# Kernel optimization log

Hardware: AMD Instinct MI355X
Metric: run time of the kernel (lower is better)

## Reference

```python
import jax, jax.numpy as jnp
import numpy as np

BN_EPS = 1e-5

def _conv1x1(x, w, b):
    # x: [B,C,H,W], w: [O,C], b: [O]
    return jnp.einsum('bchw,oc->bohw', x, w) + b[None, :, None, None]

def _maxpool2x2(x):
    B, C, H, W = x.shape
    return x.reshape(B, C, H // 2, 2, W // 2, 2).max(axis=(3, 5))

def setup_inputs() -> dict:
    key = jax.random.key(0)
    ks = jax.random.split(key, 6)
    B, C, H, W = 8, 256, 64, 64
    Ci = C // 2  # inter_channels default
    x = jax.random.normal(ks[0], (B, C, H, W), jnp.float32)
    s = lambda k, sh: jax.random.normal(k, sh, jnp.float32) * 0.02
    return {
        'x': x,
        'w_g': s(ks[1], (Ci, C)), 'b_g': jnp.zeros((Ci,), jnp.float32),
        'w_theta': s(ks[2], (Ci, C)), 'b_theta': jnp.zeros((Ci,), jnp.float32),
        'w_phi': s(ks[3], (Ci, C)), 'b_phi': jnp.zeros((Ci,), jnp.float32),
        'w_w': s(ks[4], (C, Ci)), 'b_w': jnp.zeros((C,), jnp.float32),
        'bn_gamma': 1.0 + 0.1 * jax.random.normal(ks[5], (C,), jnp.float32),
        'bn_beta': jnp.zeros((C,), jnp.float32),
    }

def reference(x, w_g, b_g, w_theta, b_theta, w_phi, b_phi, w_w, b_w, bn_gamma, bn_beta):
    B, C, H, W = x.shape
    Ci = w_g.shape[0]
    # projections (sub_sample=True: maxpool 2x2 on g and phi)
    g_x = _maxpool2x2(_conv1x1(x, w_g, b_g)).reshape(B, Ci, -1)          # [B,Ci,M]
    g_x = g_x.transpose(0, 2, 1)                                          # [B,M,Ci]
    theta_x = _conv1x1(x, w_theta, b_theta).reshape(B, Ci, -1)            # [B,Ci,N]
    theta_x = theta_x.transpose(0, 2, 1)                                  # [B,N,Ci]
    phi_x = _maxpool2x2(_conv1x1(x, w_phi, b_phi)).reshape(B, Ci, -1)     # [B,Ci,M]
    # unscaled embedded-Gaussian attention (no 1/sqrt(d), as in source)
    f = jnp.einsum('bnc,bcm->bnm', theta_x, phi_x)                        # [B,N,M]
    f_div_C = jax.nn.softmax(f, axis=-1)
    y = jnp.einsum('bnm,bmc->bnc', f_div_C, g_x)                          # [B,N,Ci]
    y = y.transpose(0, 2, 1).reshape(B, Ci, H, W)
    # W: 1x1 conv + BatchNorm (training mode: batch statistics)
    wy = _conv1x1(y, w_w, b_w)                                            # [B,C,H,W]
    mean = wy.mean(axis=(0, 2, 3), keepdims=True)
    var = wy.var(axis=(0, 2, 3), keepdims=True)
    wy = (wy - mean) * jax.lax.rsqrt(var + BN_EPS)
    wy = wy * bn_gamma[None, :, None, None] + bn_beta[None, :, None, None]
    return wy + x
```

## Files before the change

### kernel.cpp

```cpp
#include <hip/hip_runtime.h>
#include <hip/hip_bf16.h>

#define NB 8
#define NC 256
#define NCI 128
#define NSP 4096
#define NM 1024

typedef float f32x4 __attribute__((ext_vector_type(4)));
typedef float f32x16 __attribute__((ext_vector_type(16)));
typedef short s16x8 __attribute__((ext_vector_type(8)));
typedef unsigned short u16;

#define OFF_XH  (0ull)
#define OFF_XL  (16777216ull)
#define OFF_THT (33554432ull)
#define OFF_PHT (41943040ull)
#define OFF_GP  (44040192ull)
#define OFF_YH  (46137344ull)
#define OFF_YL  (54525952ull)
#define OFF_WY  (0ull)
#define OFF_WBH (62914560ull)
#define OFF_WBL (63111168ull)
#define OFF_WWH (63307776ull)
#define OFF_WWL (63373312ull)
#define OFF_S   (63438848ull)

#define GLL(src, dst) __builtin_amdgcn_global_load_lds( \
    (const __attribute__((address_space(1))) unsigned*)(src), \
    (__attribute__((address_space(3))) unsigned*)(dst), 16, 0, 0)

__device__ __forceinline__ u16 f2bf(float f) {
  union { __hip_bfloat16 h; u16 u; } v;
  v.h = __float2bfloat16(f);
  return v.u;
}
__device__ __forceinline__ float bf2f(u16 u) {
  union { unsigned u; float f; } v;
  v.u = (unsigned)u << 16;
  return v.f;
}
__device__ __forceinline__ u16 bfmax4(u16 a, u16 b, u16 c, u16 d) {
  float v = fmaxf(fmaxf(bf2f(a), bf2f(b)), fmaxf(bf2f(c), bf2f(d)));
  return f2bf(v);
}
__device__ __forceinline__ unsigned cvtpk(float lo, float hi) {
  unsigned r;
  asm volatile("v_cvt_pk_bf16_f32 %0, %1, %2" : "=v"(r) : "v"(lo), "v"(hi));
  return r;
}

__global__ void zero_stats(float* s) { s[threadIdx.x] = 0.f; }

__global__ __launch_bounds__(256) void wcvt(
    const float* __restrict__ wg, const float* __restrict__ wth,
    const float* __restrict__ wph, const float* __restrict__ ww,
    u16* __restrict__ wbh, u16* __restrict__ wbl,
    u16* __restrict__ wwh, u16* __restrict__ wwl)
{
  int idx = blockIdx.x * 256 + threadIdx.x;
  if (idx < 384 * 256) {
    int row = idx >> 8, k = idx & 255;
    float v = row < 128 ? wg[row * 256 + k]
            : row < 256 ? wth[(row - 128) * 256 + k]
                        : wph[(row - 256) * 256 + k];
    u16 h = f2bf(v);
    wbh[idx] = h;
    wbl[idx] = f2bf(v - bf2f(h));
  } else {
    int j = idx - 384 * 256;
    float v = ww[j];
    u16 h = f2bf(v);
    wwh[j] = h;
    wwl[j] = f2bf(v - bf2f(h));
  }
}

__global__ __launch_bounds__(256) void xt_cvt(const float* __restrict__ x,
                                              u16* __restrict__ xh, u16* __restrict__ xl)
{
  __shared__ float t[64 * 68];
  const int n0 = blockIdx.x << 6, c0 = blockIdx.y << 6, b = blockIdx.z;
  const int tid = threadIdx.x;
  const int cl = tid >> 4, n4 = (tid & 15) << 2;
#pragma unroll
  for (int it = 0; it < 4; ++it) {
    int c = it * 16 + cl;
    float4 v = *(const float4*)&x[((size_t)(b * NC + c0 + c)) * NSP + n0 + n4];
    *(float4*)&t[c * 68 + n4] = v;
  }
  __syncthreads();
#pragma unroll
  for (int it = 0; it < 2; ++it) {
    int task = it * 256 + tid;
    int n = task >> 3, cc = (task & 7) << 3;
    u16 oh[8], ol[8];
#pragma unroll
    for (int i = 0; i < 8; ++i) {
      float v = t[(cc + i) * 68 + n];
      oh[i] = f2bf(v);
      ol[i] = f2bf(v - bf2f(oh[i]));
    }
    size_t dst = ((size_t)(b * NSP + n0 + n)) * NC + c0 + cc;
    *(s16x8*)&xh[dst] = *(s16x8*)oh;
    *(s16x8*)&xl[dst] = *(s16x8*)ol;
  }
}

__global__ __launch_bounds__(512, 1) void proj_fused(
    const u16* __restrict__ xh, const u16* __restrict__ xl,
    const u16* __restrict__ wbh, const u16* __restrict__ wbl,
    const float* __restrict__ bg, const float* __restrict__ bth,
    const float* __restrict__ bph,
    u16* __restrict__ thT, u16* __restrict__ phT, u16* __restrict__ gp)
{
  __shared__ char smem[132608];
  u16* xsh = (u16*)smem;
  u16* xsl = (u16*)(smem + 16384);
  u16* wsh = (u16*)(smem + 32768);
  u16* wsl = (u16*)(smem + 81920);
  u16* outl = (u16*)smem;
  float* bias = (float*)(smem + 131072);

  const int b = blockIdx.y, h2 = blockIdx.x;
  const int n0 = h2 << 7;
  const int tid = threadIdx.x;
  const int wave = tid >> 6, lane = tid & 63;
  const int lo16 = lane & 15, hi4 = lane >> 4;
  const int wr = wave >> 1, wc = wave & 1;
  const int obase = wr * 96, nbase = wc * 64;

  if (tid < 384)
    bias[tid] = tid < 128 ? bg[tid] : tid < 256 ? bth[tid - 128] : bph[tid - 256];

  f32x4 acc[6][4];
#pragma unroll
  for (int i = 0; i < 6; ++i)
#pragma unroll
    for (int j = 0; j < 4; ++j) acc[i][j] = (f32x4){0.f, 0.f, 0.f, 0.f};

  for (int step = 0; step < 4; ++step) {
    __syncthreads();
#pragma unroll
    for (int i = 0; i < 2; ++i) {
      int ci = i * 512 + tid;
      int n = ci >> 3, slot = ci & 7;
      size_t rowb = ((size_t)(b * NSP + n0 + n)) * 512 + step * 128 + ((slot ^ (n & 7)) << 4);
      GLL((const char*)xh + rowb, (char*)xsh + (size_t)(i * 512 + (tid & ~63)) * 16);
      GLL((const char*)xl + rowb, (char*)xsl + (size_t)(i * 512 + (tid & ~63)) * 16);
    }
#pragma unroll
    for (int i = 0; i < 6; ++i) {
      int ci = i * 512 + tid;
      int o = ci >> 3, slot = ci & 7;
      size_t rowb = (size_t)o * 512 + step * 128 + ((slot ^ (o & 7)) << 4);
      GLL((const char*)wbh + rowb, (char*)wsh + (size_t)(i * 512 + (tid & ~63)) * 16);
      GLL((const char*)wbl + rowb, (char*)wsl + (size_t)(i * 512 + (tid & ~63)) * 16);
    }
    __syncthreads();

#pragma unroll
    for (int kc = 0; kc < 2; ++kc) {
      const int sl = kc * 4 + hi4;
      s16x8 bfh[4], bfl[4];
#pragma unroll
      for (int fn = 0; fn < 4; ++fn) {
        int n = nbase + fn * 16 + lo16;
        int off = (int)n * 128 + ((sl ^ (n & 7)) << 4);
        bfh[fn] = *(const s16x8*)((const char*)xsh + off);
        bfl[fn] = *(const s16x8*)((const char*)xsl + off);
      }
      __builtin_amdgcn_s_setprio(1);
#pragma unroll
      for (int fo = 0; fo < 6; ++fo) {
        int o = obase + fo * 16 + lo16;
        int off = (int)o * 128 + ((sl ^ (o & 7)) << 4);
        s16x8 afh = *(const s16x8*)((const char*)wsh + off);
        s16x8 afl = *(const s16x8*)((const char*)wsl + off);
#pragma unroll
        for (int fn = 0; fn < 4; ++fn) {
          acc[fo][fn] = __builtin_amdgcn_mfma_f32_16x16x32_bf16(afh, bfh[fn], acc[fo][fn], 0, 0, 0);
          acc[fo][fn] = __builtin_amdgcn_mfma_f32_16x16x32_bf16(afh, bfl[fn], acc[fo][fn], 0, 0, 0);
          acc[fo][fn] = __builtin_amdgcn_mfma_f32_16x16x32_bf16(afl, bfh[fn], acc[fo][fn], 0, 0, 0);
        }
      }
      __builtin_amdgcn_s_setprio(0);
    }
  }

  __syncthreads();
#pragma unroll
  for (int fo = 0; fo < 6; ++fo) {
    int orow = obase + fo * 16 + hi4 * 4;
    f32x4 bv = *(const f32x4*)&bias[orow];
#pragma unroll
    for (int fn = 0; fn < 4; ++fn) {
      int n = nbase + fn * 16 + lo16;
#pragma unroll
      for (int r = 0; r < 4; ++r)
        outl[(orow + r) * 137 + n] = f2bf(acc[fo][fn][r] + bv[r]);
    }
  }
  __syncthreads();

#pragma unroll
  for (int it = 0; it < 4; ++it) {
    int task = it * 512 + tid;
    int n = task >> 4, cc = (task & 15) << 3;
    u16 o[8];
#pragma unroll
    for (int i = 0; i < 8; ++i) o[i] = outl[(128 + cc + i) * 137 + n];
    *(s16x8*)&thT[((size_t)(b * NSP + n0 + n)) * NCI + cc] = *(s16x8*)o;
  }
  {
    int c = tid >> 2, wq = tid & 3;
    u16 o[8];
#pragma unroll
    for (int j = 0; j < 8; ++j) {
      int w2 = wq * 8 + j;
      o[j] = bfmax4(outl[c * 137 + 2 * w2], outl[c * 137 + 2 * w2 + 1],
                    outl[c * 137 + 64 + 2 * w2], outl[c * 137 + 64 + 2 * w2 + 1]);
    }
    *(s16x8*)&gp[((size_t)(b * NCI + c)) * NM + (h2 << 5) + wq * 8] = *(s16x8*)o;
  }
  {
    int w2 = tid >> 4, cc = (tid & 15) << 3;
    u16 o[8];
#pragma unroll
    for (int i = 0; i < 8; ++i) {
      int c = 256 + cc + i;
      o[i] = bfmax4(outl[c * 137 + 2 * w2], outl[c * 137 + 2 * w2 + 1],
                    outl[c * 137 + 64 + 2 * w2], outl[c * 137 + 64 + 2 * w2 + 1]);
    }
    *(s16x8*)&phT[((size_t)(b * NM + (h2 << 5) + w2)) * NCI + cc] = *(s16x8*)o;
  }
}

__global__ __launch_bounds__(512, 2) void attn_mfma(
    const u16* __restrict__ thT, const u16* __restrict__ phT,
    const u16* __restrict__ gP, u16* __restrict__ yh, u16* __restrict__ yl)
{
  __shared__ char smem[131072];

  const int b = blockIdx.y;
  const int n0 = blockIdx.x << 7;
  const int tid = threadIdx.x;
  const int wave = tid >> 6;
  const int qg = wave & 3;
  const int kh = wave >> 2;
  const int lane = tid & 63;
  const int l31 = lane & 31;
  const int hi1 = lane >> 5;
  const int qbase = n0 + (qg << 5);
  const int swl = (l31 & 7) << 4;

  s16x8 thb[8];
  {
    const u16* tr = &thT[((size_t)b * NSP + qbase + l31) * NCI + hi1 * 8];
#pragma unroll
    for (int kc = 0; kc < 8; ++kc) thb[kc] = *(const s16x8*)&tr[kc * 16];
  }

  f32x16 yacc[4];
#pragma unroll
  for (int ct = 0; ct < 4; ++ct) yacc[ct] = (f32x16)0.f;
  float m_i = -3e38f, l_i = 0.f;

  auto stage = [&](int s, int step) {
    char* base = smem + s * 65536;
    const int m0a = step << 6, m0b = (step + 8) << 6;
#pragma unroll
    for (int it = 0; it < 8; ++it) {
      const int rg = it >> 1;
      int r = ((it & 1) << 9) + tid;
      char* dst = base + rg * 16384 + (size_t)(((it & 1) << 9) + (tid & ~63)) * 16;
      if (rg == 0 || rg == 2) {
        int m0 = (rg == 0) ? m0a : m0b;
        int m = r >> 4, cb = (r & 15) << 4;
        const char* src = (const char*)phT + (((size_t)b * NM + m0 + m) << 8) + (cb ^ ((m & 7) << 4));
        GLL(src, dst);
      } else {
        int m0 = (rg == 1) ? m0a : m0b;
        int c = r >> 3, mb = (r & 7) << 4;
        const char* src = (const char*)gP + (((size_t)b * NCI + c) << 11) + m0 * 2 + (mb ^ ((c & 7) << 4));
        GLL(src, dst);
      }
    }
  };

  stage(0, 0);
  __syncthreads();
  int cur = 0;

  for (int step = 0; step < 8; ++step) {
    if (step < 7) stage(cur ^ 1, step + 1);
    const char* ph = smem + cur * 65536 + kh * 32768;
    const char* gg = ph + 16384;

    f32x16 s0 = (f32x16)0.f, s1 = (f32x16)0.f;
    __builtin_amdgcn_s_setprio(1);
#pragma unroll
    for (int kc = 0; kc < 8; ++kc) {
      int cofs = (kc * 32 + hi1 * 16);
      s16x8 a0 = *(const s16x8*)(ph + l31 * 256 + (cofs ^ swl));
      s16x8 a1 = *(const s16x8*)(ph + (32 + l31) * 256 + (cofs ^ swl));
      s0 = __builtin_amdgcn_mfma_f32_32x32x16_bf16(a0, thb[kc], s0, 0, 0, 0);
      s1 = __builtin_amdgcn_mfma_f32_32x32x16_bf16(a1, thb[kc], s1, 0, 0, 0);
    }
    __builtin_amdgcn_s_setprio(0);

    float pm = s0[0];
#pragma unroll
    for (int i = 1; i < 16; ++i) pm = fmaxf(pm, s0[i]);
#pragma unroll
    for (int i = 0; i < 16; ++i) pm = fmaxf(pm, s1[i]);
    pm = fmaxf(pm, __shfl_xor(pm, 32));
    float mn = fmaxf(m_i, pm);
    float sc = __expf(m_i - mn);
    float rs = 0.f;
#pragma unroll
    for (int i = 0; i < 16; ++i) { s0[i] = __expf(s0[i] - mn); rs += s0[i]; }
#pragma unroll
    for (int i = 0; i < 16; ++i) { s1[i] = __expf(s1[i] - mn); rs += s1[i]; }
    rs += __shfl_xor(rs, 32);
    l_i = l_i * sc + rs;
    m_i = mn;
#pragma unroll
    for (int ct = 0; ct < 4; ++ct)
#pragma unroll
      for (int i = 0; i < 16; ++i) yacc[ct][i] *= sc;

    s16x8 pb[4];
#pragma unroll
    for (int km = 0; km < 4; ++km) {
      int r0 = (km & 1) * 8;
      unsigned X0, X1, X2, X3;
      if (km < 2) {
        X0 = cvtpk(s0[r0 + 0], s0[r0 + 1]);
        X1 = cvtpk(s0[r0 + 2], s0[r0 + 3]);
        X2 = cvtpk(s0[r0 + 4], s0[r0 + 5]);
        X3 = cvtpk(s0[r0 + 6], s0[r0 + 7]);
      } else {
        X0 = cvtpk(s1[r0 + 0], s1[r0 + 1]);
        X1 = cvtpk(s1[r0 + 2], s1[r0 + 3]);
        X2 = cvtpk(s1[r0 + 4], s1[r0 + 5]);
        X3 = cvtpk(s1[r0 + 6], s1[r0 + 7]);
      }
      asm volatile("v_permlane32_swap_b32 %0, %1" : "+v"(X0), "+v"(X2));
      asm volatile("v_permlane32_swap_b32 %0, %1" : "+v"(X1), "+v"(X3));
      unsigned d[4] = {X0, X1, X2, X3};
      pb[km] = *(s16x8*)d;
    }

    __builtin_amdgcn_s_setprio(1);
#pragma unroll
    for (int ct = 0; ct < 4; ++ct) {
      const char* grow = gg + (ct * 32 + l31) * 128;
#pragma unroll
      for (int km = 0; km < 4; ++km) {
        s16x8 ga = *(const s16x8*)(grow + ((km * 32 + hi1 * 16) ^ swl));
        yacc[ct] = __builtin_amdgcn_mfma_f32_32x32x16_bf16(ga, pb[km], yacc[ct], 0, 0, 0);
      }
    }
    __builtin_amdgcn_s_setprio(0);

    __syncthreads();
    cur ^= 1;
  }

  float* yx = (float*)smem;
  float* ml = (float*)(smem + 65536);
  const int slot = (qg << 6) + lane;
  if (kh == 1) {
#pragma unroll
    for (int ct = 0; ct < 4; ++ct)
#pragma unroll
      for (int i4 = 0; i4 < 4; ++i4) {
        f32x4 v = {yacc[ct][i4 * 4 + 0], yacc[ct][i4 * 4 + 1],
                   yacc[ct][i4 * 4 + 2], yacc[ct][i4 * 4 + 3]};
        *(f32x4*)((char*)yx + (size_t)(((ct * 4 + i4) << 8) + slot) * 16) = v;
      }
    ml[slot * 2] = m_i;
    ml[slot * 2 + 1] = l_i;
  }
  __syncthreads();
  if (kh == 1) return;

  float m1 = ml[slot * 2], l1 = ml[slot * 2 + 1];
  float mm = fmaxf(m_i, m1);
  float sc0 = __expf(m_i - mm), sc1 = __expf(m1 - mm);
  float inv = 1.f / (l_i * sc0 + l1 * sc1);
  float a0 = sc0 * inv, a1 = sc1 * inv;
#pragma unroll
  for (int ct = 0; ct < 4; ++ct)
#pragma unroll
    for (int i4 = 0; i4 < 4; ++i4) {
      f32x4 v = *(const f32x4*)((const char*)yx + (size_t)(((ct * 4 + i4) << 8) + slot) * 16);
#pragma unroll
      for (int j = 0; j < 4; ++j)
        yacc[ct][i4 * 4 + j] = yacc[ct][i4 * 4 + j] * a0 + v[j] * a1;
    }

  u16* bounce = (u16*)(smem + 67584) + qg * 4224;
  const int qq = lane >> 1, c0 = (lane & 1) << 6;
#pragma unroll
  for (int pass = 0; pass < 2; ++pass) {
#pragma unroll
    for (int ct = 0; ct < 4; ++ct) {
#pragma unroll
      for (int rp = 0; rp < 8; ++rp) {
        int r = rp * 2;
        int c = ct * 32 + (r & 3) + 8 * (r >> 2) + 4 * hi1;
        float v0 = yacc[ct][r], v1 = yacc[ct][r + 1];
        u16 h0 = f2bf(v0), h1 = f2bf(v1);
        u16 w0 = h0, w1 = h1;
        if (pass) { w0 = f2bf(v0 - bf2f(h0)); w1 = f2bf(v1 - bf2f(h1)); }
        *(unsigned*)&bounce[l31 * 132 + c] = (unsigned)w0 | ((unsigned)w1 << 16);
      }
    }
    asm volatile("s_waitcnt lgkmcnt(0)" ::: "memory");
    u16* dst = pass ? yl : yh;
    size_t row = ((size_t)b * NSP + qbase + qq) * NCI + c0;
#pragma unroll
    for (int k = 0; k < 8; ++k)
      *(s16x8*)&dst[row + k * 8] = *(const s16x8*)&bounce[qq * 132 + c0 + k * 8];
    asm volatile("s_waitcnt lgkmcnt(0)" ::: "memory");
  }
}

__global__ __launch_bounds__(512, 1) void conv_w_mfma(
    const u16* __restrict__ yh, const u16* __restrict__ yl,
    const u16* __restrict__ wwh, const u16* __restrict__ wwl,
    const float* __restrict__ bw, float* __restrict__ wy,
    float* __restrict__ s1g, float* __restrict__ s2g)
{
  __shared__ char smem[102400];
  u16* wsh = (u16*)smem;
  u16* wsl = (u16*)(smem + 32768);
  u16* ysh = (u16*)(smem + 65536);
  u16* ysl = (u16*)(smem + 81920);
  float (*sums1)[256] = (float(*)[256])(smem + 98304);
  float (*sums2)[256] = (float(*)[256])(smem + 100352);

  const int b = blockIdx.y, n0 = blockIdx.x << 7;
  const int tid = threadIdx.x;
  const int wave = tid >> 6, lane = tid & 63;
  const int lo16 = lane & 15, hi4 = lane >> 4;
  const int wr = wave >> 1, wc = wave & 1;
  const int obase = wr * 64, nbase = wc * 64;

  f32x4 acc[4][4];
#pragma unroll
  for (int i = 0; i < 4; ++i)
#pragma unroll
    for (int j = 0; j < 4; ++j) acc[i][j] = (f32x4){0.f, 0.f, 0.f, 0.f};

  for (int step = 0; step < 2; ++step) {
    __syncthreads();
#pragma unroll
    for (int i = 0; i < 4; ++i) {
      int ci = i * 512 + tid;
      int o = ci >> 3, slot = ci & 7;
      size_t rowb = (size_t)o * 256 + step * 128 + ((slot ^ (o & 7)) << 4);
      GLL((const char*)wwh + rowb, (char*)wsh + (size_t)(i * 512 + (tid & ~63)) * 16);
      GLL((const char*)wwl + rowb, (char*)wsl + (size_t)(i * 512 + (tid & ~63)) * 16);
    }
#pragma unroll
    for (int i = 0; i < 2; ++i) {
      int ci = i * 512 + tid;
      int n = ci >> 3, slot = ci & 7;
      size_t rowb = ((size_t)(b * NSP + n0 + n)) * 256 + step * 128 + ((slot ^ (n & 7)) << 4);
      GLL((const char*)yh + rowb, (char*)ysh + (size_t)(i * 512 + (tid & ~63)) * 16);
      GLL((const char*)yl + rowb, (char*)ysl + (size_t)(i * 512 + (tid & ~63)) * 16);
    }
    __syncthreads();

#pragma unroll
    for (int kc = 0; kc < 2; ++kc) {
      const int sl = kc * 4 + hi4;
      s16x8 bfh[4], bfl[4];
#pragma unroll
      for (int fn = 0; fn < 4; ++fn) {
        int n = nbase + fn * 16 + lo16;
        int off = (int)n * 128 + ((sl ^ (n & 7)) << 4);
        bfh[fn] = *(const s16x8*)((const char*)ysh + off);
        bfl[fn] = *(const s16x8*)((const char*)ysl + off);
      }
      __builtin_amdgcn_s_setprio(1);
#pragma unroll
      for (int fo = 0; fo < 4; ++fo) {
        int o = obase + fo * 16 + lo16;
        int off = (int)o * 128 + ((sl ^ (o & 7)) << 4);
        s16x8 afh = *(const s16x8*)((const char*)wsh + off);
        s16x8 afl = *(const s16x8*)((const char*)wsl + off);
#pragma unroll
        for (int fn = 0; fn < 4; ++fn) {
          acc[fo][fn] = __builtin_amdgcn_mfma_f32_16x16x32_bf16(afh, bfh[fn], acc[fo][fn], 0, 0, 0);
          acc[fo][fn] = __builtin_amdgcn_mfma_f32_16x16x32_bf16(afh, bfl[fn], acc[fo][fn], 0, 0, 0);
          acc[fo][fn] = __builtin_amdgcn_mfma_f32_16x16x32_bf16(afl, bfh[fn], acc[fo][fn], 0, 0, 0);
        }
      }
      __builtin_amdgcn_s_setprio(0);
    }
  }

#pragma unroll
  for (int fo = 0; fo < 4; ++fo) {
    int orow = obase + fo * 16 + hi4 * 4;
    float bv[4];
#pragma unroll
    for (int r = 0; r < 4; ++r) bv[r] = bw[orow + r];
    float ss[4] = {0.f, 0.f, 0.f, 0.f}, sq[4] = {0.f, 0.f, 0.f, 0.f};
#pragma unroll
    for (int fn = 0; fn < 4; ++fn) {
      int col = n0 + nbase + fn * 16 + lo16;
#pragma unroll
      for (int r = 0; r < 4; ++r) {
        float v = acc[fo][fn][r] + bv[r];
        wy[((size_t)(b * NC) + orow + r) * NSP + col] = v;
        ss[r] += v;
        sq[r] += v * v;
      }
    }
#pragma unroll
    for (int r = 0; r < 4; ++r) {
#pragma unroll
      for (int d = 1; d < 16; d <<= 1) {
        ss[r] += __shfl_xor(ss[r], d);
        sq[r] += __shfl_xor(sq[r], d);
      }
    }
    if (lo16 == 0) {
#pragma unroll
      for (int r = 0; r < 4; ++r) {
        sums1[wc][orow + r] = ss[r];
        sums2[wc][orow + r] = sq[r];
      }
    }
  }
  __syncthreads();
  if (tid < 256) {
    atomicAdd(&s1g[tid], sums1[0][tid] + sums1[1][tid]);
    atomicAdd(&s2g[tid], sums2[0][tid] + sums2[1][tid]);
  }
}

__global__ __launch_bounds__(256) void bn_res4(
    const float* __restrict__ wy, const float* __restrict__ x,
    const float* __restrict__ s1, const float* __restrict__ s2,
    const float* __restrict__ gamma, const float* __restrict__ beta,
    float* __restrict__ out)
{
  int i4 = (blockIdx.x * 256 + threadIdx.x) << 2;
  int c = (i4 >> 12) & 255;
  const float cnt = 1.f / 32768.f;
  float mean = s1[c] * cnt;
  float var = s2[c] * cnt - mean * mean;
  float inv = rsqrtf(var + 1e-5f) * gamma[c];
  float bet = beta[c];
  float4 w = *(const float4*)&wy[i4];
  float4 xv = *(const float4*)&x[i4];
  float4 o;
  o.x = (w.x - mean) * inv + bet + xv.x;
  o.y = (w.y - mean) * inv + bet + xv.y;
  o.z = (w.z - mean) * inv + bet + xv.z;
  o.w = (w.w - mean) * inv + bet + xv.w;
  *(float4*)&out[i4] = o;
}

extern "C" void kernel_launch(void* const* d_in, const int* in_sizes, int n_in,
                              void* d_out, int out_size, void* d_ws, size_t ws_size,
                              hipStream_t stream) {
  const float* x    = (const float*)d_in[0];
  const float* w_g  = (const float*)d_in[1];
  const float* b_g  = (const float*)d_in[2];
  const float* w_th = (const float*)d_in[3];
  const float* b_th = (const float*)d_in[4];
  const float* w_ph = (const float*)d_in[5];
  const float* b_ph = (const float*)d_in[6];
  const float* w_w  = (const float*)d_in[7];
  const float* b_w  = (const float*)d_in[8];
  const float* gam  = (const float*)d_in[9];
  const float* bet  = (const float*)d_in[10];
  float* out = (float*)d_out;
  char* ws = (char*)d_ws;

  u16*   xh  = (u16*)(ws + OFF_XH);
  u16*   xl  = (u16*)(ws + OFF_XL);
  u16*   thT = (u16*)(ws + OFF_THT);
  u16*   phT = (u16*)(ws + OFF_PHT);
  u16*   gp  = (u16*)(ws + OFF_GP);
  u16*   yhb = (u16*)(ws + OFF_YH);
  u16*   ylb = (u16*)(ws + OFF_YL);
  float* wy  = (float*)(ws + OFF_WY);
  u16*   wbh = (u16*)(ws + OFF_WBH);
  u16*   wbl = (u16*)(ws + OFF_WBL);
  u16*   wwh = (u16*)(ws + OFF_WWH);
  u16*   wwl = (u16*)(ws + OFF_WWL);
  float* s1  = (float*)(ws + OFF_S);
  float* s2  = s1 + 256;

  wcvt<<<dim3(512), 256, 0, stream>>>(w_g, w_th, w_ph, w_w, wbh, wbl, wwh, wwl);
  zero_stats<<<dim3(1), 512, 0, stream>>>(s1);
  xt_cvt<<<dim3(64, 4, 8), 256, 0, stream>>>(x, xh, xl);

  proj_fused<<<dim3(32, 8), 512, 0, stream>>>(xh, xl, wbh, wbl, b_g, b_th, b_ph, thT, phT, gp);

  attn_mfma<<<dim3(32, 8), 512, 0, stream>>>(thT, phT, gp, yhb, ylb);

  conv_w_mfma<<<dim3(32, 8), 512, 0, stream>>>(yhb, ylb, wwh, wwl, b_w, wy, s1, s2);

  bn_res4<<<dim3(8192), 256, 0, stream>>>(wy, x, s1, s2, gam, bet, out);
}
```

Baseline: 112.0 us.

## Split attention key range across four waves per query group with tree merge

After: 138.6 us. +23.7%, slower.

```diff
diff --git a/kernel.cpp b/kernel.cpp
--- a/kernel.cpp
+++ b/kernel.cpp
@@ -236,11 +236,11 @@
   }
 }
 
-__global__ __launch_bounds__(512, 2) void attn_mfma(
+__global__ __launch_bounds__(1024, 4) void attn_mfma(
     const u16* __restrict__ thT, const u16* __restrict__ phT,
     const u16* __restrict__ gP, u16* __restrict__ yh, u16* __restrict__ yl)
 {
-  __shared__ char smem[131072];
+  __shared__ char smem[135168];
 
   const int b = blockIdx.y;
   const int n0 = blockIdx.x << 7;
@@ -253,6 +253,7 @@
   const int hi1 = lane >> 5;
   const int qbase = n0 + (qg << 5);
   const int swl = (l31 & 7) << 4;
+  const int gsw = ((l31 >> 1) & 3) << 4;
 
   s16x8 thb[8];
   {
@@ -268,22 +269,19 @@
 
   auto stage = [&](int s, int step) {
     char* base = smem + s * 65536;
-    const int m0a = step << 6, m0b = (step + 8) << 6;
-#pragma unroll
-    for (int it = 0; it < 8; ++it) {
-      const int rg = it >> 1;
-      int r = ((it & 1) << 9) + tid;
-      char* dst = base + rg * 16384 + (size_t)(((it & 1) << 9) + (tid & ~63)) * 16;
-      if (rg == 0 || rg == 2) {
-        int m0 = (rg == 0) ? m0a : m0b;
-        int m = r >> 4, cb = (r & 15) << 4;
+#pragma unroll
+    for (int it = 0; it < 4; ++it) {
+      const int m0 = (it * 8 + step) << 5;
+      char* reg = base + it * 16384;
+      if (tid < 512) {
+        int m = tid >> 4, cb = (tid & 15) << 4;
         const char* src = (const char*)phT + (((size_t)b * NM + m0 + m) << 8) + (cb ^ ((m & 7) << 4));
-        GLL(src, dst);
+        GLL(src, reg + (size_t)(tid & ~63) * 16);
       } else {
-        int m0 = (rg == 1) ? m0a : m0b;
-        int c = r >> 3, mb = (r & 7) << 4;
-        const char* src = (const char*)gP + (((size_t)b * NCI + c) << 11) + m0 * 2 + (mb ^ ((c & 7) << 4));
-        GLL(src, dst);
+        int c2 = tid - 512;
+        int c = c2 >> 2, mb = (c2 & 3) << 4;
+        const char* src = (const char*)gP + (((size_t)b * NCI + c) << 11) + m0 * 2 + (mb ^ (((c >> 1) & 3) << 4));
+        GLL(src, reg + 8192 + (size_t)(c2 & ~63) * 16);
       }
     }
   };
@@ -294,34 +292,27 @@
 
   for (int step = 0; step < 8; ++step) {
     if (step < 7) stage(cur ^ 1, step + 1);
-    const char* ph = smem + cur * 65536 + kh * 32768;
-    const char* gg = ph + 16384;
-
-    f32x16 s0 = (f32x16)0.f, s1 = (f32x16)0.f;
+    const char* ph = smem + cur * 65536 + kh * 16384;
+    const char* gg = ph + 8192;
+
+    f32x16 s0 = (f32x16)0.f;
     __builtin_amdgcn_s_setprio(1);
 #pragma unroll
     for (int kc = 0; kc < 8; ++kc) {
-      int cofs = (kc * 32 + hi1 * 16);
-      s16x8 a0 = *(const s16x8*)(ph + l31 * 256 + (cofs ^ swl));
-      s16x8 a1 = *(const s16x8*)(ph + (32 + l31) * 256 + (cofs ^ swl));
+      s16x8 a0 = *(const s16x8*)(ph + l31 * 256 + ((kc * 32 + hi1 * 16) ^ swl));
       s0 = __builtin_amdgcn_mfma_f32_32x32x16_bf16(a0, thb[kc], s0, 0, 0, 0);
-      s1 = __builtin_amdgcn_mfma_f32_32x32x16_bf16(a1, thb[kc], s1, 0, 0, 0);
     }
     __builtin_amdgcn_s_setprio(0);
 
     float pm = s0[0];
 #pragma unroll
     for (int i = 1; i < 16; ++i) pm = fmaxf(pm, s0[i]);
-#pragma unroll
-    for (int i = 0; i < 16; ++i) pm = fmaxf(pm, s1[i]);
     pm = fmaxf(pm, __shfl_xor(pm, 32));
     float mn = fmaxf(m_i, pm);
     float sc = __expf(m_i - mn);
     float rs = 0.f;
 #pragma unroll
     for (int i = 0; i < 16; ++i) { s0[i] = __expf(s0[i] - mn); rs += s0[i]; }
-#pragma unroll
-    for (int i = 0; i < 16; ++i) { s1[i] = __expf(s1[i] - mn); rs += s1[i]; }
     rs += __shfl_xor(rs, 32);
     l_i = l_i * sc + rs;
     m_i = mn;
@@ -330,22 +321,14 @@
 #pragma unroll
       for (int i = 0; i < 16; ++i) yacc[ct][i] *= sc;
 
-    s16x8 pb[4];
-#pragma unroll
-    for (int km = 0; km < 4; ++km) {
-      int r0 = (km & 1) * 8;
-      unsigned X0, X1, X2, X3;
-      if (km < 2) {
-        X0 = cvtpk(s0[r0 + 0], s0[r0 + 1]);
-        X1 = cvtpk(s0[r0 + 2], s0[r0 + 3]);
-        X2 = cvtpk(s0[r0 + 4], s0[r0 + 5]);
-        X3 = cvtpk(s0[r0 + 6], s0[r0 + 7]);
-      } else {
-        X0 = cvtpk(s1[r0 + 0], s1[r0 + 1]);
-        X1 = cvtpk(s1[r0 + 2], s1[r0 + 3]);
-        X2 = cvtpk(s1[r0 + 4], s1[r0 + 5]);
-        X3 = cvtpk(s1[r0 + 6], s1[r0 + 7]);
-      }
+    s16x8 pb[2];
+#pragma unroll
+    for (int km = 0; km < 2; ++km) {
+      int r0 = km * 8;
+      unsigned X0 = cvtpk(s0[r0 + 0], s0[r0 + 1]);
+      unsigned X1 = cvtpk(s0[r0 + 2], s0[r0 + 3]);
+      unsigned X2 = cvtpk(s0[r0 + 4], s0[r0 + 5]);
+      unsigned X3 = cvtpk(s0[r0 + 6], s0[r0 + 7]);
       asm volatile("v_permlane32_swap_b32 %0, %1" : "+v"(X0), "+v"(X2));
       asm volatile("v_permlane32_swap_b32 %0, %1" : "+v"(X1), "+v"(X3));
       unsigned d[4] = {X0, X1, X2, X3};
@@ -355,10 +338,10 @@
     __builtin_amdgcn_s_setprio(1);
 #pragma unroll
     for (int ct = 0; ct < 4; ++ct) {
-      const char* grow = gg + (ct * 32 + l31) * 128;
-#pragma unroll
-      for (int km = 0; km < 4; ++km) {
-        s16x8 ga = *(const s16x8*)(grow + ((km * 32 + hi1 * 16) ^ swl));
+      const char* grow = gg + (ct * 32 + l31) * 64;
+#pragma unroll
+      for (int km = 0; km < 2; ++km) {
+        s16x8 ga = *(const s16x8*)(grow + ((km * 32 + hi1 * 16) ^ gsw));
         yacc[ct] = __builtin_amdgcn_mfma_f32_32x32x16_bf16(ga, pb[km], yacc[ct], 0, 0, 0);
       }
     }
@@ -368,10 +351,13 @@
     cur ^= 1;
   }
 
-  float* yx = (float*)smem;
-  float* ml = (float*)(smem + 65536);
+  float* yxA = (float*)smem;
+  float* yxB = (float*)(smem + 65536);
+  float* mlA = (float*)(smem + 131072);
+  float* mlB = (float*)(smem + 133120);
   const int slot = (qg << 6) + lane;
-  if (kh == 1) {
+
+  auto deposit = [&](float* yx, float* ml) {
 #pragma unroll
     for (int ct = 0; ct < 4; ++ct)
 #pragma unroll
@@ -382,26 +368,42 @@
       }
     ml[slot * 2] = m_i;
     ml[slot * 2 + 1] = l_i;
-  }
-  __syncthreads();
-  if (kh == 1) return;
-
-  float m1 = ml[slot * 2], l1 = ml[slot * 2 + 1];
-  float mm = fmaxf(m_i, m1);
-  float sc0 = __expf(m_i - mm), sc1 = __expf(m1 - mm);
-  float inv = 1.f / (l_i * sc0 + l1 * sc1);
-  float a0 = sc0 * inv, a1 = sc1 * inv;
+  };
+  auto mergein = [&](const float* yx, const float* ml) {
+    float m1 = ml[slot * 2], l1 = ml[slot * 2 + 1];
+    float mm = fmaxf(m_i, m1);
+    float sc0 = __expf(m_i - mm), sc1 = __expf(m1 - mm);
+    l_i = l_i * sc0 + l1 * sc1;
+    m_i = mm;
+#pragma unroll
+    for (int ct = 0; ct < 4; ++ct)
+#pragma unroll
+      for (int i4 = 0; i4 < 4; ++i4) {
+        f32x4 v = *(const f32x4*)((const char*)yx + (size_t)(((ct * 4 + i4) << 8) + slot) * 16);
+#pragma unroll
+        for (int j = 0; j < 4; ++j)
+          yacc[ct][i4 * 4 + j] = yacc[ct][i4 * 4 + j] * sc0 + v[j] * sc1;
+      }
+  };
+
+  if (kh == 2) deposit(yxA, mlA);
+  if (kh == 3) deposit(yxB, mlB);
+  __syncthreads();
+  if (kh == 0) mergein(yxA, mlA);
+  if (kh == 1) mergein(yxB, mlB);
+  __syncthreads();
+  if (kh == 1) deposit(yxA, mlA);
+  __syncthreads();
+  if (kh >= 1) return;
+  mergein(yxA, mlA);
+
+  float inv = 1.f / l_i;
 #pragma unroll
   for (int ct = 0; ct < 4; ++ct)
 #pragma unroll
-    for (int i4 = 0; i4 < 4; ++i4) {
-      f32x4 v = *(const f32x4*)((const char*)yx + (size_t)(((ct * 4 + i4) << 8) + slot) * 16);
-#pragma unroll
-      for (int j = 0; j < 4; ++j)
-        yacc[ct][i4 * 4 + j] = yacc[ct][i4 * 4 + j] * a0 + v[j] * a1;
-    }
-
-  u16* bounce = (u16*)(smem + 67584) + qg * 4224;
+    for (int i = 0; i < 16; ++i) yacc[ct][i] *= inv;
+
+  u16* bounce = (u16*)(smem + 65536) + qg * 4224;
   const int qq = lane >> 1, c0 = (lane & 1) << 6;
 #pragma unroll
   for (int pass = 0; pass < 2; ++pass) {
@@ -606,7 +608,7 @@
 
   proj_fused<<<dim3(32, 8), 512, 0, stream>>>(xh, xl, wbh, wbl, b_g, b_th, b_ph, thT, phT, gp);
 
-  attn_mfma<<<dim3(32, 8), 512, 0, stream>>>(thT, phT, gp, yhb, ylb);
+  attn_mfma<<<dim3(32, 8), 1024, 0, stream>>>(thT, phT, gp, yhb, ylb);
 
   conv_w_mfma<<<dim3(32, 8), 512, 0, stream>>>(yhb, ylb, wwh, wwl, b_w, wy, s1, s2);
 
```
